# Kernel tuning notes

Hardware: AMD Instinct MI355X
Metric: run time of the kernel (lower is better)

The kernel has to match this reference:

```python
import math
import jax, jax.numpy as jnp
import numpy as np

S = 32.0
M1 = 1.0
M2 = 0.5
M3 = 0.0
MM = M2 * math.sin(math.pi - M2)
NUM_CLASSES = 100000
FEATURES = 512
BATCH = 512


def setup_inputs() -> dict:
    key = jax.random.key(0)
    k1, k2, k3 = jax.random.split(key, 3)
    inputs = jax.random.normal(k1, (BATCH, FEATURES), dtype=jnp.float32)
    labels = jax.random.randint(k2, (BATCH,), 0, NUM_CLASSES, dtype=jnp.int64)
    # xavier_uniform on [num_classes, features]
    limit = math.sqrt(6.0 / (NUM_CLASSES + FEATURES))
    weight = jax.random.uniform(k3, (NUM_CLASSES, FEATURES), minval=-limit, maxval=limit, dtype=jnp.float32)
    return {"inputs": inputs, "labels": labels, "weight": weight}


def reference(inputs, labels, weight):
    # L2 normalize (torch F.normalize uses eps=1e-12 clamp on norm)
    inp_n = inputs / jnp.maximum(jnp.linalg.norm(inputs, axis=1, keepdims=True), 1e-12)
    w_n = weight / jnp.maximum(jnp.linalg.norm(weight, axis=1, keepdims=True), 1e-12)
    cos_in = jnp.clip(inp_n @ w_n.T, -1.0 + 1e-6, 1.0 - 1e-6)  # [N, C]
    theta_in = jnp.arccos(cos_in)
    one_hot = jax.nn.one_hot(labels, NUM_CLASSES, dtype=cos_in.dtype)
    theta_out = theta_in + (theta_in * (M1 - 1.0) + M2) * one_hot
    cos_out = jnp.where(
        theta_out < math.pi,
        jnp.cos(theta_out) - M3 * one_hot,
        cos_in - MM * one_hot - M3 * one_hot,
    )
    outs = S * cos_out  # [N, C]
    # mean cross-entropy
    logp = jax.nn.log_softmax(outs, axis=1)
    n = jnp.arange(BATCH)
    loss = -jnp.mean(logp[n, labels])
    target_cos_in = cos_in[n, labels][:, None]
    target_theta_in = theta_in[n, labels][:, None]
    target_cos_out = cos_out[n, labels][:, None]
    return loss, outs, target_cos_in, target_theta_in, target_cos_out
```

## Files before the change

### kernel.cpp

```cpp
#include <hip/hip_runtime.h>
#include <stdint.h>

#define BATCH 512
#define FEAT 512
#define NCLS 100000
#define BM 128
#define BN 128
#define BK 64
#define NBLK_N 782
#define NCHUNK (NBLK_N * 2)
#define SCALE_S 32.0f
#define MARGIN 0.5f
#define MM_CONST 0.23971276930210156f
#define PI_F 3.14159265358979f

typedef unsigned int u32;
typedef unsigned short u16;
typedef __bf16 bf16x8 __attribute__((ext_vector_type(8)));
typedef float f32x4 __attribute__((ext_vector_type(4)));

__device__ __forceinline__ u16 f2bf(float f) {
  u32 u = __float_as_uint(f);
  u += 0x7fffu + ((u >> 16) & 1u);
  return (u16)(u >> 16);
}

__device__ __forceinline__ void async_copy16(const void* g, void* l) {
  __builtin_amdgcn_global_load_lds((const __attribute__((address_space(1))) u32*)g,
                                   (__attribute__((address_space(3))) u32*)l,
                                   16, 0, 0);
}

__device__ __forceinline__ float block_reduce_sum(float v, float* sbuf) {
  for (int off = 1; off < 64; off <<= 1) v += __shfl_xor(v, off, 64);
  int wid = threadIdx.x >> 6, lane = threadIdx.x & 63;
  __syncthreads();
  if (lane == 0) sbuf[wid] = v;
  __syncthreads();
  return sbuf[0] + sbuf[1] + sbuf[2] + sbuf[3];
}

__global__ __launch_bounds__(256) void norm_rows_kernel(const float* __restrict__ src,
                                                        u16* __restrict__ dst, int nrows) {
  int row = (blockIdx.x << 2) + (threadIdx.x >> 6);
  int lane = threadIdx.x & 63;
  if (row >= nrows) return;
  const float4* p = (const float4*)(src + (size_t)row * FEAT);
  float4 a = p[lane], b = p[lane + 64];
  float ss = a.x * a.x + a.y * a.y + a.z * a.z + a.w * a.w +
             b.x * b.x + b.y * b.y + b.z * b.z + b.w * b.w;
#pragma unroll
  for (int off = 1; off < 64; off <<= 1) ss += __shfl_xor(ss, off, 64);
  float inv = 1.0f / fmaxf(sqrtf(ss), 1e-12f);
  u32 o0 = (u32)f2bf(a.x * inv) | ((u32)f2bf(a.y * inv) << 16);
  u32 o1 = (u32)f2bf(a.z * inv) | ((u32)f2bf(a.w * inv) << 16);
  u32 o2 = (u32)f2bf(b.x * inv) | ((u32)f2bf(b.y * inv) << 16);
  u32 o3 = (u32)f2bf(b.z * inv) | ((u32)f2bf(b.w * inv) << 16);
  uint2* d = (uint2*)(dst + (size_t)row * FEAT);
  d[lane] = make_uint2(o0, o1);
  d[lane + 64] = make_uint2(o2, o3);
}

__global__ __launch_bounds__(256) void gemm_kernel(const u16* __restrict__ A,
                                                   const u16* __restrict__ B,
                                                   const int* __restrict__ labels,
                                                   float* __restrict__ outs,
                                                   float* __restrict__ partials) {
  __shared__ __align__(16) u16 sA[BM * BK];
  __shared__ __align__(16) u16 sB[BN * BK];

  const int tid = threadIdx.x;
  const int lane = tid & 63;
  const int wid = tid >> 6;
  const int waveM = wid >> 1, waveN = wid & 1;
  const int bm = blockIdx.x, bn = blockIdx.y;
  const int quad = lane >> 4, l15 = lane & 15;

  int srow[4], scb[4];
#pragma unroll
  for (int rd = 0; rd < 4; ++rd) {
    int idx = rd * 256 + tid;
    int r = idx >> 3;
    srow[rd] = r;
    scb[rd] = (idx & 7) ^ (r & 7);
  }

  f32x4 acc[4][4] = {};

  for (int kt = 0; kt < FEAT / BK; ++kt) {
#pragma unroll
    for (int rd = 0; rd < 4; ++rd) {
      int r = srow[rd], cb = scb[rd];
      const u16* ga = A + (size_t)(bm * BM + r) * FEAT + kt * BK + cb * 8;
      int brow = bn * BN + r;
      if (brow >= NCLS) brow = NCLS - 1;
      const u16* gb = B + (size_t)brow * FEAT + kt * BK + cb * 8;
      int li = (rd * 256 + tid) * 8;
      async_copy16(ga, &sA[li]);
      async_copy16(gb, &sB[li]);
    }
    __syncthreads();
#pragma unroll
    for (int ks = 0; ks < 2; ++ks) {
      int j0 = ks * 4 + quad;
      bf16x8 aF[4], bF[4];
#pragma unroll
      for (int mi = 0; mi < 4; ++mi) {
        int r = waveM * 64 + mi * 16 + l15;
        aF[mi] = *(const bf16x8*)&sA[(r * 8 + (j0 ^ (r & 7))) * 8];
      }
#pragma unroll
      for (int ni = 0; ni < 4; ++ni) {
        int r = waveN * 64 + ni * 16 + l15;
        bF[ni] = *(const bf16x8*)&sB[(r * 8 + (j0 ^ (r & 7))) * 8];
      }
#pragma unroll
      for (int mi = 0; mi < 4; ++mi)
#pragma unroll
        for (int ni = 0; ni < 4; ++ni)
          acc[mi][ni] = __builtin_amdgcn_mfma_f32_16x16x32_bf16(aF[mi], bF[ni],
                                                                acc[mi][ni], 0, 0, 0);
    }
    __syncthreads();
  }

#pragma unroll
  for (int mi = 0; mi < 4; ++mi) {
#pragma unroll
    for (int reg = 0; reg < 4; ++reg) {
      int rloc = waveM * 64 + mi * 16 + quad * 4 + reg;
      int rg = bm * BM + rloc;
      int lab = labels[rg];
      float vals[4];
      float rmax = -1e30f;
#pragma unroll
      for (int ni = 0; ni < 4; ++ni) {
        int cg = bn * BN + waveN * 64 + ni * 16 + l15;
        float v = acc[mi][ni][reg];
        v = fminf(fmaxf(v, -1.0f + 1e-6f), 1.0f - 1e-6f);
        if (cg == lab) {
          float th = acosf(v) + MARGIN;
          v = (th < PI_F) ? cosf(th) : (v - MM_CONST);
        }
        v *= SCALE_S;
        if (cg < NCLS)
          outs[(size_t)rg * NCLS + cg] = v;
        else
          v = -1e30f;
        vals[ni] = v;
        rmax = fmaxf(rmax, v);
      }
#pragma unroll
      for (int off = 1; off < 16; off <<= 1) rmax = fmaxf(rmax, __shfl_xor(rmax, off, 64));
      float rsum = 0.f;
#pragma unroll
      for (int ni = 0; ni < 4; ++ni) rsum += __expf(vals[ni] - rmax);
#pragma unroll
      for (int off = 1; off < 16; off <<= 1) rsum += __shfl_xor(rsum, off, 64);
      if (l15 == 0) {
        float* p = partials + ((size_t)rg * NCHUNK + (bn * 2 + waveN)) * 2;
        p[0] = rmax;
        p[1] = rsum;
      }
    }
  }
}

__global__ __launch_bounds__(256) void combine_kernel(const float* __restrict__ partials,
                                                      const float* __restrict__ outs,
                                                      const int* __restrict__ labels,
                                                      float* __restrict__ loss_r) {
  int r = blockIdx.x, tid = threadIdx.x;
  const float* p = partials + (size_t)r * NCHUNK * 2;
  float m = -1e30f, l = 0.f;
  for (int i = tid; i < NCHUNK; i += 256) {
    float mi = p[2 * i], li = p[2 * i + 1];
    if (mi > m) { l = l * __expf(m - mi) + li; m = mi; }
    else l += li * __expf(mi - m);
  }
  for (int off = 1; off < 64; off <<= 1) {
    float mo = __shfl_xor(m, off, 64);
    float lo = __shfl_xor(l, off, 64);
    if (mo > m) { l = l * __expf(m - mo) + lo; m = mo; }
    else l += lo * __expf(mo - m);
  }
  __shared__ float sm[4], sl[4];
  int wv = tid >> 6, lane = tid & 63;
  if (lane == 0) { sm[wv] = m; sl[wv] = l; }
  __syncthreads();
  if (tid == 0) {
    for (int w = 1; w < 4; ++w) {
      float mo = sm[w], lo = sl[w];
      if (mo > m) { l = l * __expf(m - mo) + lo; m = mo; }
      else l += lo * __expf(mo - m);
    }
    float lse = m + logf(l);
    loss_r[r] = lse - outs[(size_t)r * NCLS + labels[r]];
  }
}

__global__ __launch_bounds__(256) void loss_kernel(const float* __restrict__ loss_r,
                                                   float* __restrict__ out0) {
  __shared__ float sbuf[4];
  float v = loss_r[threadIdx.x] + loss_r[threadIdx.x + 256];
  float s = block_reduce_sum(v, sbuf);
  if (threadIdx.x == 0) out0[0] = s * (1.0f / BATCH);
}

__global__ __launch_bounds__(256) void targets_kernel(const float* __restrict__ inputs,
                                                      const int* __restrict__ labels,
                                                      const float* __restrict__ weight,
                                                      float* __restrict__ tdst) {
  __shared__ float sbuf[4];
  int r = blockIdx.x, t = threadIdx.x;
  int lab = labels[r];
  const float2* px = (const float2*)(inputs + (size_t)r * FEAT);
  const float2* pw = (const float2*)(weight + (size_t)lab * FEAT);
  float2 x = px[t], w = pw[t];
  float dot = block_reduce_sum(x.x * w.x + x.y * w.y, sbuf);
  float sx = block_reduce_sum(x.x * x.x + x.y * x.y, sbuf);
  float sw = block_reduce_sum(w.x * w.x + w.y * w.y, sbuf);
  if (t == 0) {
    float inv = 1.0f / (fmaxf(sqrtf(sx), 1e-12f) * fmaxf(sqrtf(sw), 1e-12f));
    float ci = fminf(fmaxf(dot * inv, -1.0f + 1e-6f), 1.0f - 1e-6f);
    float th = acosf(ci);
    float t2 = th + MARGIN;
    float co = (t2 < PI_F) ? cosf(t2) : (ci - MM_CONST);
    tdst[r] = ci;
    tdst[BATCH + r] = th;
    tdst[2 * BATCH + r] = co;
  }
}

extern "C" void kernel_launch(void* const* d_in, const int* in_sizes, int n_in,
                              void* d_out, int out_size, void* d_ws, size_t ws_size,
                              hipStream_t stream) {
  const float* inputs = (const float*)d_in[0];
  const int* labels = (const int*)d_in[1];
  const float* weight = (const float*)d_in[2];
  float* out = (float*)d_out;
  float* outs = out + 1;
  float* tdst = out + 1 + (size_t)BATCH * NCLS;

  char* ws = (char*)d_ws;
  u16* wsA = (u16*)ws;
  u16* wsB = (u16*)(ws + 524288);
  float* partials = (float*)(ws + 524288 + 102400000);
  float* loss_r = (float*)(ws + 524288 + 102400000 + (size_t)BATCH * NCHUNK * 2 * 4);

  norm_rows_kernel<<<BATCH / 4, 256, 0, stream>>>(inputs, wsA, BATCH);
  norm_rows_kernel<<<(NCLS + 3) / 4, 256, 0, stream>>>(weight, wsB, NCLS);
  gemm_kernel<<<dim3(BATCH / BM, NBLK_N), 256, 0, stream>>>(wsA, wsB, labels, outs, partials);
  combine_kernel<<<BATCH, 256, 0, stream>>>(partials, outs, labels, loss_r);
  loss_kernel<<<1, 256, 0, stream>>>(loss_r, out);
  targets_kernel<<<BATCH, 256, 0, stream>>>(inputs, labels, weight, tdst);
}
```

Baseline: 577.3 us.

## Load GEMM fragments directly from global memory and remap blocks for L2 reuse

Removes the LDS staging path (async global-to-LDS copies plus barriers) from the GEMM and has each lane load its bf16 MFMA fragments straight from global memory, fully unrolled over K. The grid is flattened to 1D and remapped so groups of 8 column blocks share the 4 row blocks, making B tiles reused across concurrently running blocks via L2. This cuts barrier and LDS traffic, but each wave now reissues redundant global loads that used to be shared through LDS, and it relies on cache hits to hold up bandwidth.

```diff
diff --git a/kernel.cpp b/kernel.cpp
--- a/kernel.cpp
+++ b/kernel.cpp
@@ -6,7 +6,6 @@
 #define NCLS 100000
 #define BM 128
 #define BN 128
-#define BK 64
 #define NBLK_N 782
 #define NCHUNK (NBLK_N * 2)
 #define SCALE_S 32.0f
@@ -23,12 +22,6 @@
   u32 u = __float_as_uint(f);
   u += 0x7fffu + ((u >> 16) & 1u);
   return (u16)(u >> 16);
-}
-
-__device__ __forceinline__ void async_copy16(const void* g, void* l) {
-  __builtin_amdgcn_global_load_lds((const __attribute__((address_space(1))) u32*)g,
-                                   (__attribute__((address_space(3))) u32*)l,
-                                   16, 0, 0);
 }
 
 __device__ __forceinline__ float block_reduce_sum(float v, float* sbuf) {
@@ -66,62 +59,46 @@
                                                    const int* __restrict__ labels,
                                                    float* __restrict__ outs,
                                                    float* __restrict__ partials) {
-  __shared__ __align__(16) u16 sA[BM * BK];
-  __shared__ __align__(16) u16 sB[BN * BK];
+  const int L = blockIdx.x;
+  const int bn = (L >> 5) * 8 + (L & 7);
+  const int bm = (L >> 3) & 3;
+  if (bn >= NBLK_N) return;
 
   const int tid = threadIdx.x;
   const int lane = tid & 63;
   const int wid = tid >> 6;
   const int waveM = wid >> 1, waveN = wid & 1;
-  const int bm = blockIdx.x, bn = blockIdx.y;
   const int quad = lane >> 4, l15 = lane & 15;
 
-  int srow[4], scb[4];
-#pragma unroll
-  for (int rd = 0; rd < 4; ++rd) {
-    int idx = rd * 256 + tid;
-    int r = idx >> 3;
-    srow[rd] = r;
-    scb[rd] = (idx & 7) ^ (r & 7);
+  const u16* aPtr[4];
+  const u16* bPtr[4];
+#pragma unroll
+  for (int mi = 0; mi < 4; ++mi) {
+    int ra = bm * BM + waveM * 64 + mi * 16 + l15;
+    aPtr[mi] = A + (size_t)ra * FEAT + quad * 8;
+  }
+#pragma unroll
+  for (int ni = 0; ni < 4; ++ni) {
+    int rb = bn * BN + waveN * 64 + ni * 16 + l15;
+    if (rb >= NCLS) rb = NCLS - 1;
+    bPtr[ni] = B + (size_t)rb * FEAT + quad * 8;
   }
 
   f32x4 acc[4][4] = {};
 
-  for (int kt = 0; kt < FEAT / BK; ++kt) {
-#pragma unroll
-    for (int rd = 0; rd < 4; ++rd) {
-      int r = srow[rd], cb = scb[rd];
-      const u16* ga = A + (size_t)(bm * BM + r) * FEAT + kt * BK + cb * 8;
-      int brow = bn * BN + r;
-      if (brow >= NCLS) brow = NCLS - 1;
-      const u16* gb = B + (size_t)brow * FEAT + kt * BK + cb * 8;
-      int li = (rd * 256 + tid) * 8;
-      async_copy16(ga, &sA[li]);
-      async_copy16(gb, &sB[li]);
-    }
-    __syncthreads();
-#pragma unroll
-    for (int ks = 0; ks < 2; ++ks) {
-      int j0 = ks * 4 + quad;
-      bf16x8 aF[4], bF[4];
-#pragma unroll
-      for (int mi = 0; mi < 4; ++mi) {
-        int r = waveM * 64 + mi * 16 + l15;
-        aF[mi] = *(const bf16x8*)&sA[(r * 8 + (j0 ^ (r & 7))) * 8];
-      }
-#pragma unroll
-      for (int ni = 0; ni < 4; ++ni) {
-        int r = waveN * 64 + ni * 16 + l15;
-        bF[ni] = *(const bf16x8*)&sB[(r * 8 + (j0 ^ (r & 7))) * 8];
-      }
-#pragma unroll
-      for (int mi = 0; mi < 4; ++mi)
-#pragma unroll
-        for (int ni = 0; ni < 4; ++ni)
-          acc[mi][ni] = __builtin_amdgcn_mfma_f32_16x16x32_bf16(aF[mi], bF[ni],
-                                                                acc[mi][ni], 0, 0, 0);
-    }
-    __syncthreads();
+#pragma unroll
+  for (int kt = 0; kt < FEAT / 32; ++kt) {
+    bf16x8 aF[4], bF[4];
+#pragma unroll
+    for (int mi = 0; mi < 4; ++mi) aF[mi] = *(const bf16x8*)(aPtr[mi] + kt * 32);
+#pragma unroll
+    for (int ni = 0; ni < 4; ++ni) bF[ni] = *(const bf16x8*)(bPtr[ni] + kt * 32);
+#pragma unroll
+    for (int mi = 0; mi < 4; ++mi)
+#pragma unroll
+      for (int ni = 0; ni < 4; ++ni)
+        acc[mi][ni] = __builtin_amdgcn_mfma_f32_16x16x32_bf16(aF[mi], bF[ni],
+                                                              acc[mi][ni], 0, 0, 0);
   }
 
 #pragma unroll
@@ -250,7 +227,7 @@
 
   norm_rows_kernel<<<BATCH / 4, 256, 0, stream>>>(inputs, wsA, BATCH);
   norm_rows_kernel<<<(NCLS + 3) / 4, 256, 0, stream>>>(weight, wsB, NCLS);
-  gemm_kernel<<<dim3(BATCH / BM, NBLK_N), 256, 0, stream>>>(wsA, wsB, labels, outs, partials);
+  gemm_kernel<<<98 * 32, 256, 0, stream>>>(wsA, wsB, labels, outs, partials);
   combine_kernel<<<BATCH, 256, 0, stream>>>(partials, outs, labels, loss_r);
   loss_kernel<<<1, 256, 0, stream>>>(loss_r, out);
   targets_kernel<<<BATCH, 256, 0, stream>>>(inputs, labels, weight, tdst);
```

After: 593.5 us. +2.8%, slower.
